# Kernel optimization log

Hardware: AMD Instinct MI355X
Metric: run time of the kernel (lower is better)

Reference implementation:

```python
import jax, jax.numpy as jnp
import numpy as np

N_NODES = 50000


def gcn_conv(h, src, dst, W, b, n):
    # PyG GCNConv: x' = D^{-1/2} (A + I) D^{-1/2} (h W) + b
    x = h @ W  # [N, out]
    deg = jax.ops.segment_sum(jnp.ones_like(src, dtype=x.dtype), dst, num_segments=n) + 1.0  # self-loop
    dis = deg ** -0.5
    norm = dis[src] * dis[dst]  # [E]
    msg = x[src] * norm[:, None]  # [E, out]
    agg = jax.ops.segment_sum(msg, dst, num_segments=n)
    agg = agg + x * (dis * dis)[:, None]  # self-loop term: 1/deg_i * x_i
    return agg + b


def setup_inputs() -> dict:
    key = jax.random.key(0)
    ks = jax.random.split(key, 8)
    n, e = N_NODES, 800000
    d_in, d_rni, h = 128, 32, 256
    x = jax.random.normal(ks[0], (n, d_in), dtype=jnp.float32)
    rni = jax.random.normal(ks[1], (n, d_rni), dtype=jnp.float32)
    edge_index = jax.random.randint(ks[2], (2, e), 0, n, dtype=jnp.int64)
    s1 = (d_in + d_rni) ** -0.5
    s2 = h ** -0.5
    W1 = jax.random.normal(ks[3], (d_in + d_rni, h), dtype=jnp.float32) * s1
    b1 = jnp.zeros((h,), dtype=jnp.float32)
    W2 = jax.random.normal(ks[4], (h, h), dtype=jnp.float32) * s2
    b2 = jnp.zeros((h,), dtype=jnp.float32)
    W_out = jax.random.normal(ks[5], (h, h), dtype=jnp.float32) * s2
    b_out = jnp.zeros((h,), dtype=jnp.float32)
    return {"x": x, "rni": rni, "edge_index": edge_index, "W1": W1, "b1": b1,
            "W2": W2, "b2": b2, "W_out": W_out, "b_out": b_out}


def reference(x, rni, edge_index, W1, b1, W2, b2, W_out, b_out):
    n = x.shape[0]
    src, dst = edge_index[0], edge_index[1]
    h = jnp.concatenate([x, rni], axis=-1)  # RNI concat
    h = jax.nn.relu(gcn_conv(h, src, dst, W1, b1, n))
    h = jax.nn.relu(gcn_conv(h, src, dst, W2, b2, n))
    return h @ W_out + b_out
```

## Files before the change

kernel.cpp:

```cpp
#include <hip/hip_runtime.h>
#include <hip/hip_bf16.h>
#include <hip/hip_fp16.h>
#include <math.h>

#define D_IN   128
#define D_RNI  32
#define HID    256

typedef _Float16 half8 __attribute__((ext_vector_type(8)));
typedef float    f32x4 __attribute__((ext_vector_type(4)));

__global__ void k_detect(const unsigned int* __restrict__ w, int nwords, int* __restrict__ mode) {
    __shared__ unsigned int red[256];
    unsigned int acc = 0;
    for (int i = threadIdx.x; i < 1024; i += 256) {
        int idx = 2 * i + 1;
        if (idx < nwords) acc |= w[idx];
    }
    red[threadIdx.x] = acc;
    __syncthreads();
    for (int s = 128; s > 0; s >>= 1) {
        if (threadIdx.x < s) red[threadIdx.x] |= red[threadIdx.x + s];
        __syncthreads();
    }
    if (threadIdx.x == 0) *mode = (red[0] == 0u) ? 1 : 0;
}

__global__ void k_count(const unsigned int* __restrict__ ew, const int* __restrict__ mode_p,
                        int* __restrict__ counts, int e) {
    int mode = *mode_p;
    int i = blockIdx.x * 256 + threadIdx.x;
    if (i >= e) return;
    int d = mode ? (int)ew[2 * ((size_t)e + i)] : (int)ew[(size_t)e + i];
    atomicAdd(&counts[d], 1);
}

__global__ __launch_bounds__(1024) void k_scan1(const int* __restrict__ counts,
                                                int* __restrict__ incl,
                                                int* __restrict__ bsum, int n) {
    __shared__ int sd[1024];
    int t = threadIdx.x;
    int i = blockIdx.x * 1024 + t;
    int v = (i < n) ? counts[i] : 0;
    sd[t] = v;
    __syncthreads();
    for (int off = 1; off < 1024; off <<= 1) {
        int tmp = (t >= off) ? sd[t - off] : 0;
        __syncthreads();
        sd[t] += tmp;
        __syncthreads();
    }
    if (i < n) incl[i] = sd[t];
    if (t == 1023) bsum[blockIdx.x] = sd[1023];
}

__global__ __launch_bounds__(1024) void k_scan2(int* __restrict__ bsum, int nb) {
    __shared__ int sd[1024];
    int t = threadIdx.x;
    int v = (t < nb) ? bsum[t] : 0;
    sd[t] = v;
    __syncthreads();
    for (int off = 1; off < 1024; off <<= 1) {
        int tmp = (t >= off) ? sd[t - off] : 0;
        __syncthreads();
        sd[t] += tmp;
        __syncthreads();
    }
    if (t < nb) bsum[t] = sd[t] - v;
    if (t == nb - 1) bsum[nb] = sd[t];
}

__global__ void k_scan3(const int* __restrict__ counts, const int* __restrict__ incl,
                        const int* __restrict__ bsum,
                        int* __restrict__ rowptr, int* __restrict__ cursor,
                        float* __restrict__ dis, int n, int nb) {
    int i = blockIdx.x * 256 + threadIdx.x;
    if (i >= n) return;
    int excl = incl[i] - counts[i] + bsum[i >> 10];
    rowptr[i] = excl;
    cursor[i] = excl;
    dis[i] = 1.0f / sqrtf((float)(counts[i] + 1));
    if (i == 0) rowptr[n] = bsum[nb];
}

__global__ void k_scatter(const unsigned int* __restrict__ ew, const int* __restrict__ mode_p,
                          int* __restrict__ cursor, int* __restrict__ csr, int e) {
    int mode = *mode_p;
    int i = blockIdx.x * 256 + threadIdx.x;
    if (i >= e) return;
    int s, d;
    if (mode) {
        s = (int)ew[2 * (size_t)i];
        d = (int)ew[2 * ((size_t)e + i)];
    } else {
        s = (int)ew[(size_t)i];
        d = (int)ew[(size_t)e + i];
    }
    int pos = atomicAdd(&cursor[d], 1);
    csr[pos] = s;
}

__global__ void k_cvt_wt(const float* __restrict__ W, __half* __restrict__ Wt,
                         int K, int N, int total) {
    int i = blockIdx.x * 256 + threadIdx.x;
    if (i >= total) return;
    int k = i / N, nn = i - k * N;
    Wt[(size_t)nn * K + k] = __float2half(W[i]);
}

#define KT 32
#define LSTR 40
template <bool A_F32, bool ADD_BIAS, bool HALF_OUT>
__global__ __launch_bounds__(512) void k_mgemm(const void* __restrict__ Av, int strideA, int KA,
                                               const void* __restrict__ A2v, int strideA2,
                                               const __half* __restrict__ Bt,
                                               const float* __restrict__ bias,
                                               void* Cv, int M, int K) {
    __shared__ __half As[128 * LSTR];
    __shared__ __half Bs[256 * LSTR];
    int tid = threadIdx.x;
    int wave = tid >> 6, lane = tid & 63;
    int wm = wave >> 2, wn = wave & 3;
    int q = lane >> 4, m16 = lane & 15;
    int r0 = blockIdx.x * 128;

    int ar  = tid >> 2, akq = (tid & 3) * 8;
    int br  = tid >> 1, bkq = (tid & 1) * 16;

    int arow = r0 + ar; if (arow >= M) arow = M - 1;

    f32x4 acc[4][4] = {};

    float4 afr0, afr1;
    uint4  areg;
    uint4  breg0, breg1;

    auto loadA = [&](int k0) {
        if (A_F32) {
            const float* src; int stride, kk0;
            if (k0 < KA) { src = (const float*)Av;  stride = strideA;  kk0 = k0; }
            else         { src = (const float*)A2v; stride = strideA2; kk0 = k0 - KA; }
            const float* p = &src[(size_t)arow * stride + kk0 + akq];
            afr0 = *reinterpret_cast<const float4*>(p);
            afr1 = *reinterpret_cast<const float4*>(p + 4);
        } else {
            const __half* src = (const __half*)Av;
            areg = *reinterpret_cast<const uint4*>(&src[(size_t)arow * strideA + k0 + akq]);
        }
    };
    auto loadB = [&](int k0) {
        const __half* p = &Bt[(size_t)br * K + k0 + bkq];
        breg0 = *reinterpret_cast<const uint4*>(p);
        breg1 = *reinterpret_cast<const uint4*>(p + 8);
    };
    auto writeLDS = [&]() {
        if (A_F32) {
            union { __half2 h2[4]; uint4 u; } uu;
            uu.h2[0] = __floats2half2_rn(afr0.x, afr0.y);
            uu.h2[1] = __floats2half2_rn(afr0.z, afr0.w);
            uu.h2[2] = __floats2half2_rn(afr1.x, afr1.y);
            uu.h2[3] = __floats2half2_rn(afr1.z, afr1.w);
            *reinterpret_cast<uint4*>(&As[ar * LSTR + akq]) = uu.u;
        } else {
            *reinterpret_cast<uint4*>(&As[ar * LSTR + akq]) = areg;
        }
        *reinterpret_cast<uint4*>(&Bs[br * LSTR + bkq])     = breg0;
        *reinterpret_cast<uint4*>(&Bs[br * LSTR + bkq + 8]) = breg1;
    };

    loadA(0); loadB(0);
    for (int k0 = 0; k0 < K; k0 += KT) {
        __syncthreads();
        writeLDS();
        __syncthreads();
        if (k0 + KT < K) { loadA(k0 + KT); loadB(k0 + KT); }

        half8 af[4], bf[4];
        #pragma unroll
        for (int mi = 0; mi < 4; ++mi)
            af[mi] = *reinterpret_cast<const half8*>(&As[(wm * 64 + mi * 16 + m16) * LSTR + q * 8]);
        #pragma unroll
        for (int ni = 0; ni < 4; ++ni)
            bf[ni] = *reinterpret_cast<const half8*>(&Bs[(wn * 64 + ni * 16 + m16) * LSTR + q * 8]);
        #pragma unroll
        for (int mi = 0; mi < 4; ++mi)
            #pragma unroll
            for (int ni = 0; ni < 4; ++ni)
                acc[mi][ni] = __builtin_amdgcn_mfma_f32_16x16x32_f16(af[mi], bf[ni], acc[mi][ni], 0, 0, 0);
    }

    #pragma unroll
    for (int mi = 0; mi < 4; ++mi) {
        #pragma unroll
        for (int r = 0; r < 4; ++r) {
            int row = r0 + wm * 64 + mi * 16 + q * 4 + r;
            if (row >= M) continue;
            #pragma unroll
            for (int ni = 0; ni < 4; ++ni) {
                int col = wn * 64 + ni * 16 + m16;
                float v = acc[mi][ni][r];
                if (ADD_BIAS) v += bias[col];
                if (HALF_OUT) ((__half*)Cv)[(size_t)row * HID + col] = __float2half(v);
                else          ((float*)Cv)[(size_t)row * HID + col] = v;
            }
        }
    }
}

__global__ __launch_bounds__(256) void k_agg(const __half* __restrict__ xh,
                                             const int* __restrict__ rowptr,
                                             const int* __restrict__ csr,
                                             const float* __restrict__ dis,
                                             const float* __restrict__ bias,
                                             __half* __restrict__ outh, int n) {
    int i = blockIdx.x * 4 + (threadIdx.x >> 6);
    if (i >= n) return;
    int lane = threadIdx.x & 63;
    int c4 = lane * 4;
    float disd = dis[i];
    int e0 = rowptr[i], e1 = rowptr[i + 1];

    float acc0, acc1, acc2, acc3;
    {
        uint2 v = *reinterpret_cast<const uint2*>(&xh[(size_t)i * HID + c4]);
        float2 f0 = __half22float2(*reinterpret_cast<__half2*>(&v.x));
        float2 f1 = __half22float2(*reinterpret_cast<__half2*>(&v.y));
        float ws = disd * disd;
        acc0 = f0.x * ws; acc1 = f0.y * ws; acc2 = f1.x * ws; acc3 = f1.y * ws;
    }

    for (int e = e0; e < e1; e += 64) {
        int cnt = min(64, e1 - e);
        int sreg = 0; float wreg = 0.0f;
        if (lane < cnt) {
            sreg = csr[e + lane];
            wreg = dis[sreg] * disd;
        }
        int j = 0;
        for (; j + 4 <= cnt; j += 4) {
            int   s0 = __shfl(sreg, j + 0), s1 = __shfl(sreg, j + 1);
            int   s2 = __shfl(sreg, j + 2), s3 = __shfl(sreg, j + 3);
            float w0 = __shfl(wreg, j + 0), w1 = __shfl(wreg, j + 1);
            float w2 = __shfl(wreg, j + 2), w3 = __shfl(wreg, j + 3);
            uint2 v0 = *reinterpret_cast<const uint2*>(&xh[(size_t)s0 * HID + c4]);
            uint2 v1 = *reinterpret_cast<const uint2*>(&xh[(size_t)s1 * HID + c4]);
            uint2 v2 = *reinterpret_cast<const uint2*>(&xh[(size_t)s2 * HID + c4]);
            uint2 v3 = *reinterpret_cast<const uint2*>(&xh[(size_t)s3 * HID + c4]);
            float2 a0 = __half22float2(*reinterpret_cast<__half2*>(&v0.x));
            float2 b0 = __half22float2(*reinterpret_cast<__half2*>(&v0.y));
            float2 a1 = __half22float2(*reinterpret_cast<__half2*>(&v1.x));
            float2 b1 = __half22float2(*reinterpret_cast<__half2*>(&v1.y));
            float2 a2 = __half22float2(*reinterpret_cast<__half2*>(&v2.x));
            float2 b2 = __half22float2(*reinterpret_cast<__half2*>(&v2.y));
            float2 a3 = __half22float2(*reinterpret_cast<__half2*>(&v3.x));
            float2 b3 = __half22float2(*reinterpret_cast<__half2*>(&v3.y));
            acc0 = fmaf(a0.x, w0, acc0); acc1 = fmaf(a0.y, w0, acc1);
            acc2 = fmaf(b0.x, w0, acc2); acc3 = fmaf(b0.y, w0, acc3);
            acc0 = fmaf(a1.x, w1, acc0); acc1 = fmaf(a1.y, w1, acc1);
            acc2 = fmaf(b1.x, w1, acc2); acc3 = fmaf(b1.y, w1, acc3);
            acc0 = fmaf(a2.x, w2, acc0); acc1 = fmaf(a2.y, w2, acc1);
            acc2 = fmaf(b2.x, w2, acc2); acc3 = fmaf(b2.y, w2, acc3);
            acc0 = fmaf(a3.x, w3, acc0); acc1 = fmaf(a3.y, w3, acc1);
            acc2 = fmaf(b3.x, w3, acc2); acc3 = fmaf(b3.y, w3, acc3);
        }
        for (; j < cnt; ++j) {
            int   s = __shfl(sreg, j);
            float w = __shfl(wreg, j);
            uint2 v = *reinterpret_cast<const uint2*>(&xh[(size_t)s * HID + c4]);
            float2 a = __half22float2(*reinterpret_cast<__half2*>(&v.x));
            float2 b = __half22float2(*reinterpret_cast<__half2*>(&v.y));
            acc0 = fmaf(a.x, w, acc0); acc1 = fmaf(a.y, w, acc1);
            acc2 = fmaf(b.x, w, acc2); acc3 = fmaf(b.y, w, acc3);
        }
    }

    float4 bb = *reinterpret_cast<const float4*>(&bias[c4]);
    union { __half2 h2[2]; uint2 u; } o;
    o.h2[0] = __floats2half2_rn(fmaxf(acc0 + bb.x, 0.0f), fmaxf(acc1 + bb.y, 0.0f));
    o.h2[1] = __floats2half2_rn(fmaxf(acc2 + bb.z, 0.0f), fmaxf(acc3 + bb.w, 0.0f));
    *reinterpret_cast<uint2*>(&outh[(size_t)i * HID + c4]) = o.u;
}

extern "C" void kernel_launch(void* const* d_in, const int* in_sizes, int n_in,
                              void* d_out, int out_size, void* d_ws, size_t ws_size,
                              hipStream_t stream) {
    const float* x     = (const float*)d_in[0];
    const float* rni   = (const float*)d_in[1];
    const unsigned int* ew = (const unsigned int*)d_in[2];
    const float* W1    = (const float*)d_in[3];
    const float* b1    = (const float*)d_in[4];
    const float* W2    = (const float*)d_in[5];
    const float* b2    = (const float*)d_in[6];
    const float* W_out = (const float*)d_in[7];
    const float* b_out = (const float*)d_in[8];
    float* out = (float*)d_out;

    const int n  = in_sizes[0] / D_IN;
    const int e  = in_sizes[2] / 2;
    const int nb = (n + 1023) / 1024;
    const int K1 = D_IN + D_RNI;

    char* ws = (char*)d_ws;
    size_t off = 0;
    auto carve = [&](size_t bytes) {
        char* p = ws + off;
        off = (off + bytes + 255) & ~(size_t)255;
        return p;
    };
    __half* xh    = (__half*)carve((size_t)n * HID * sizeof(__half));
    __half* h     = (__half*)carve((size_t)n * HID * sizeof(__half));
    __half* W1t   = (__half*)carve((size_t)K1 * HID * sizeof(__half));
    __half* W2t   = (__half*)carve((size_t)HID * HID * sizeof(__half));
    __half* Wot   = (__half*)carve((size_t)HID * HID * sizeof(__half));
    int*   counts = (int*)carve((size_t)n * sizeof(int));
    int*   incl   = (int*)carve((size_t)n * sizeof(int));
    int*   bsum   = (int*)carve((size_t)(nb + 1) * sizeof(int));
    int*   rowptr = (int*)carve((size_t)(n + 1) * sizeof(int));
    int*   cursor = (int*)carve((size_t)n * sizeof(int));
    float* dis    = (float*)carve((size_t)n * sizeof(float));
    int*   csr    = (int*)carve((size_t)e * sizeof(int));
    int*   mode   = (int*)carve(sizeof(int));
    (void)ws_size;

    const int eb = (e + 255) / 256;
    const int gemm_blocks = (n + 127) / 128;
    const int agg_blocks  = (n + 3) / 4;

    k_detect<<<1, 256, 0, stream>>>(ew, 2 * e, mode);
    hipMemsetAsync(counts, 0, (size_t)n * sizeof(int), stream);
    k_count<<<eb, 256, 0, stream>>>(ew, mode, counts, e);
    k_scan1<<<nb, 1024, 0, stream>>>(counts, incl, bsum, n);
    k_scan2<<<1, 1024, 0, stream>>>(bsum, nb);
    k_scan3<<<(n + 255) / 256, 256, 0, stream>>>(counts, incl, bsum, rowptr, cursor, dis, n, nb);
    k_scatter<<<eb, 256, 0, stream>>>(ew, mode, cursor, csr, e);

    {
        int tw1 = K1 * HID;
        k_cvt_wt<<<(tw1 + 255) / 256, 256, 0, stream>>>(W1, W1t, K1, HID, tw1);
        int tw = HID * HID;
        k_cvt_wt<<<(tw + 255) / 256, 256, 0, stream>>>(W2, W2t, HID, HID, tw);
        k_cvt_wt<<<(tw + 255) / 256, 256, 0, stream>>>(W_out, Wot, HID, HID, tw);
    }

    k_mgemm<true, false, true><<<gemm_blocks, 512, 0, stream>>>(x, D_IN, D_IN, rni, D_RNI,
                                                                W1t, nullptr, xh, n, K1);
    k_agg<<<agg_blocks, 256, 0, stream>>>(xh, rowptr, csr, dis, b1, h, n);

    k_mgemm<false, false, true><<<gemm_blocks, 512, 0, stream>>>(h, HID, HID, nullptr, 0,
                                                                 W2t, nullptr, xh, n, HID);
    k_agg<<<agg_blocks, 256, 0, stream>>>(xh, rowptr, csr, dis, b2, h, n);

    k_mgemm<false, true, false><<<gemm_blocks, 512, 0, stream>>>(h, HID, HID, nullptr, 0,
                                                                 Wot, b_out, out, n, HID);
}
```

Baseline: 368.3 us.

## Merge prep kernels, fold block-sum scan into scan3, double-buffer GEMM LDS

Detection and the three weight-conversion kernels are merged into one launch. The separate block-sum scan kernel is removed, and each scan3 block now recomputes its prefix over the block sums with wave shuffles. The GEMM gets double-buffered LDS with a single barrier per K step and a launch-bounds occupancy hint. Together these cut launch count and GEMM synchronisation, at the cost of doubled LDS use and redundant per-block prefix work. The wave-level block-sum prefix only handles up to 64 block sums.

New measurement: 361.4 us. About the same (-1.9%).

```diff
diff --git a/kernel.cpp b/kernel.cpp
--- a/kernel.cpp
+++ b/kernel.cpp
@@ -10,20 +10,42 @@
 typedef _Float16 half8 __attribute__((ext_vector_type(8)));
 typedef float    f32x4 __attribute__((ext_vector_type(4)));
 
-__global__ void k_detect(const unsigned int* __restrict__ w, int nwords, int* __restrict__ mode) {
-    __shared__ unsigned int red[256];
-    unsigned int acc = 0;
-    for (int i = threadIdx.x; i < 1024; i += 256) {
-        int idx = 2 * i + 1;
-        if (idx < nwords) acc |= w[idx];
-    }
-    red[threadIdx.x] = acc;
-    __syncthreads();
-    for (int s = 128; s > 0; s >>= 1) {
-        if (threadIdx.x < s) red[threadIdx.x] |= red[threadIdx.x + s];
+__global__ void k_prep(const unsigned int* __restrict__ ew, int nwords, int* __restrict__ mode,
+                       const float* __restrict__ W1, __half* __restrict__ W1t,
+                       const float* __restrict__ W2, __half* __restrict__ W2t,
+                       const float* __restrict__ Wo, __half* __restrict__ Wot) {
+    int b = blockIdx.x;
+    if (b == 0) {
+        __shared__ unsigned int red[256];
+        unsigned int acc = 0;
+        for (int i = threadIdx.x; i < 1024; i += 256) {
+            int idx = 2 * i + 1;
+            if (idx < nwords) acc |= ew[idx];
+        }
+        red[threadIdx.x] = acc;
         __syncthreads();
-    }
-    if (threadIdx.x == 0) *mode = (red[0] == 0u) ? 1 : 0;
+        for (int s = 128; s > 0; s >>= 1) {
+            if (threadIdx.x < s) red[threadIdx.x] |= red[threadIdx.x + s];
+            __syncthreads();
+        }
+        if (threadIdx.x == 0) *mode = (red[0] == 0u) ? 1 : 0;
+        return;
+    }
+    int i = (b - 1) * 256 + threadIdx.x;
+    const int T1 = (D_IN + D_RNI) * HID;
+    const int T2 = HID * HID;
+    if (i < T1) {
+        int k = i / HID, nn = i - k * HID;
+        W1t[(size_t)nn * (D_IN + D_RNI) + k] = __float2half(W1[i]);
+    } else if (i < T1 + T2) {
+        int j = i - T1;
+        int k = j / HID, nn = j - k * HID;
+        W2t[(size_t)nn * HID + k] = __float2half(W2[j]);
+    } else {
+        int j = i - T1 - T2;
+        int k = j / HID, nn = j - k * HID;
+        Wot[(size_t)nn * HID + k] = __float2half(Wo[j]);
+    }
 }
 
 __global__ void k_count(const unsigned int* __restrict__ ew, const int* __restrict__ mode_p,
@@ -54,33 +76,32 @@
     if (t == 1023) bsum[blockIdx.x] = sd[1023];
 }
 
-__global__ __launch_bounds__(1024) void k_scan2(int* __restrict__ bsum, int nb) {
-    __shared__ int sd[1024];
-    int t = threadIdx.x;
-    int v = (t < nb) ? bsum[t] : 0;
-    sd[t] = v;
-    __syncthreads();
-    for (int off = 1; off < 1024; off <<= 1) {
-        int tmp = (t >= off) ? sd[t - off] : 0;
-        __syncthreads();
-        sd[t] += tmp;
-        __syncthreads();
-    }
-    if (t < nb) bsum[t] = sd[t] - v;
-    if (t == nb - 1) bsum[nb] = sd[t];
-}
-
 __global__ void k_scan3(const int* __restrict__ counts, const int* __restrict__ incl,
                         const int* __restrict__ bsum,
                         int* __restrict__ rowptr, int* __restrict__ cursor,
                         float* __restrict__ dis, int n, int nb) {
-    int i = blockIdx.x * 256 + threadIdx.x;
+    __shared__ int pre_s, tot_s;
+    int t = threadIdx.x;
+    int c = (blockIdx.x * 256) >> 10;
+    if (t < 64) {
+        int v   = (t < nb) ? bsum[t] : 0;
+        int pre = (t < c)  ? v : 0;
+        int tot = v;
+        #pragma unroll
+        for (int m = 32; m > 0; m >>= 1) {
+            pre += __shfl_down(pre, m);
+            tot += __shfl_down(tot, m);
+        }
+        if (t == 0) { pre_s = pre; tot_s = tot; }
+    }
+    __syncthreads();
+    int i = blockIdx.x * 256 + t;
     if (i >= n) return;
-    int excl = incl[i] - counts[i] + bsum[i >> 10];
+    int excl = incl[i] - counts[i] + pre_s;
     rowptr[i] = excl;
     cursor[i] = excl;
     dis[i] = 1.0f / sqrtf((float)(counts[i] + 1));
-    if (i == 0) rowptr[n] = bsum[nb];
+    if (i == 0) rowptr[n] = tot_s;
 }
 
 __global__ void k_scatter(const unsigned int* __restrict__ ew, const int* __restrict__ mode_p,
@@ -100,24 +121,16 @@
     csr[pos] = s;
 }
 
-__global__ void k_cvt_wt(const float* __restrict__ W, __half* __restrict__ Wt,
-                         int K, int N, int total) {
-    int i = blockIdx.x * 256 + threadIdx.x;
-    if (i >= total) return;
-    int k = i / N, nn = i - k * N;
-    Wt[(size_t)nn * K + k] = __float2half(W[i]);
-}
-
 #define KT 32
 #define LSTR 40
 template <bool A_F32, bool ADD_BIAS, bool HALF_OUT>
-__global__ __launch_bounds__(512) void k_mgemm(const void* __restrict__ Av, int strideA, int KA,
-                                               const void* __restrict__ A2v, int strideA2,
-                                               const __half* __restrict__ Bt,
-                                               const float* __restrict__ bias,
-                                               void* Cv, int M, int K) {
-    __shared__ __half As[128 * LSTR];
-    __shared__ __half Bs[256 * LSTR];
+__global__ __launch_bounds__(512, 4) void k_mgemm(const void* __restrict__ Av, int strideA, int KA,
+                                                  const void* __restrict__ A2v, int strideA2,
+                                                  const __half* __restrict__ Bt,
+                                                  const float* __restrict__ bias,
+                                                  void* Cv, int M, int K) {
+    __shared__ __half As[2][128 * LSTR];
+    __shared__ __half Bs[2][256 * LSTR];
     int tid = threadIdx.x;
     int wave = tid >> 6, lane = tid & 63;
     int wm = wave >> 2, wn = wave & 3;
@@ -153,40 +166,45 @@
         breg0 = *reinterpret_cast<const uint4*>(p);
         breg1 = *reinterpret_cast<const uint4*>(p + 8);
     };
-    auto writeLDS = [&]() {
+    auto writeLDS = [&](int buf) {
         if (A_F32) {
             union { __half2 h2[4]; uint4 u; } uu;
             uu.h2[0] = __floats2half2_rn(afr0.x, afr0.y);
             uu.h2[1] = __floats2half2_rn(afr0.z, afr0.w);
             uu.h2[2] = __floats2half2_rn(afr1.x, afr1.y);
             uu.h2[3] = __floats2half2_rn(afr1.z, afr1.w);
-            *reinterpret_cast<uint4*>(&As[ar * LSTR + akq]) = uu.u;
+            *reinterpret_cast<uint4*>(&As[buf][ar * LSTR + akq]) = uu.u;
         } else {
-            *reinterpret_cast<uint4*>(&As[ar * LSTR + akq]) = areg;
-        }
-        *reinterpret_cast<uint4*>(&Bs[br * LSTR + bkq])     = breg0;
-        *reinterpret_cast<uint4*>(&Bs[br * LSTR + bkq + 8]) = breg1;
+            *reinterpret_cast<uint4*>(&As[buf][ar * LSTR + akq]) = areg;
+        }
+        *reinterpret_cast<uint4*>(&Bs[buf][br * LSTR + bkq])     = breg0;
+        *reinterpret_cast<uint4*>(&Bs[buf][br * LSTR + bkq + 8]) = breg1;
     };
 
+    const int S = K / KT;
     loadA(0); loadB(0);
-    for (int k0 = 0; k0 < K; k0 += KT) {
-        __syncthreads();
-        writeLDS();
-        __syncthreads();
-        if (k0 + KT < K) { loadA(k0 + KT); loadB(k0 + KT); }
+    writeLDS(0);
+    __syncthreads();
+
+    for (int t = 0; t < S; ++t) {
+        int cur = t & 1;
+        if (t + 1 < S) { loadA((t + 1) * KT); loadB((t + 1) * KT); }
 
         half8 af[4], bf[4];
         #pragma unroll
         for (int mi = 0; mi < 4; ++mi)
-            af[mi] = *reinterpret_cast<const half8*>(&As[(wm * 64 + mi * 16 + m16) * LSTR + q * 8]);
+            af[mi] = *reinterpret_cast<const half8*>(&As[cur][(wm * 64 + mi * 16 + m16) * LSTR + q * 8]);
         #pragma unroll
         for (int ni = 0; ni < 4; ++ni)
-            bf[ni] = *reinterpret_cast<const half8*>(&Bs[(wn * 64 + ni * 16 + m16) * LSTR + q * 8]);
+            bf[ni] = *reinterpret_cast<const half8*>(&Bs[cur][(wn * 64 + ni * 16 + m16) * LSTR + q * 8]);
         #pragma unroll
         for (int mi = 0; mi < 4; ++mi)
             #pragma unroll
             for (int ni = 0; ni < 4; ++ni)
                 acc[mi][ni] = __builtin_amdgcn_mfma_f32_16x16x32_f16(af[mi], bf[ni], acc[mi][ni], 0, 0, 0);
+
+        if (t + 1 < S) writeLDS(cur ^ 1);
+        __syncthreads();
     }
 
     #pragma unroll
@@ -325,22 +343,14 @@
     const int eb = (e + 255) / 256;
     const int gemm_blocks = (n + 127) / 128;
     const int agg_blocks  = (n + 3) / 4;
-
-    k_detect<<<1, 256, 0, stream>>>(ew, 2 * e, mode);
+    const int prep_blocks = 1 + (K1 * HID + 2 * HID * HID + 255) / 256;
+
+    k_prep<<<prep_blocks, 256, 0, stream>>>(ew, 2 * e, mode, W1, W1t, W2, W2t, W_out, Wot);
     hipMemsetAsync(counts, 0, (size_t)n * sizeof(int), stream);
     k_count<<<eb, 256, 0, stream>>>(ew, mode, counts, e);
     k_scan1<<<nb, 1024, 0, stream>>>(counts, incl, bsum, n);
-    k_scan2<<<1, 1024, 0, stream>>>(bsum, nb);
     k_scan3<<<(n + 255) / 256, 256, 0, stream>>>(counts, incl, bsum, rowptr, cursor, dis, n, nb);
     k_scatter<<<eb, 256, 0, stream>>>(ew, mode, cursor, csr, e);
-
-    {
-        int tw1 = K1 * HID;
-        k_cvt_wt<<<(tw1 + 255) / 256, 256, 0, stream>>>(W1, W1t, K1, HID, tw1);
-        int tw = HID * HID;
-        k_cvt_wt<<<(tw + 255) / 256, 256, 0, stream>>>(W2, W2t, HID, HID, tw);
-        k_cvt_wt<<<(tw + 255) / 256, 256, 0, stream>>>(W_out, Wot, HID, HID, tw);
-    }
 
     k_mgemm<true, false, true><<<gemm_blocks, 512, 0, stream>>>(x, D_IN, D_IN, rni, D_RNI,
                                                                 W1t, nullptr, xh, n, K1);
```
